# Kernel tuning notes

Hardware: AMD Instinct MI355X
Metric: run time of the kernel (lower is better)

The kernel has to match this reference:

```python
import jax, jax.numpy as jnp
import numpy as np

H = 256
K = 16
EPS_LN = 1e-5


def setup_inputs() -> dict:
    key = jax.random.key(0)
    ks = jax.random.split(key, 24)
    B, N = 64, 256
    s = lambda *sh: 1.0 / np.sqrt(sh[0])
    inp = {
        "feat": jax.random.normal(ks[0], (B, N, H), jnp.float32),
        "centers": jax.random.normal(ks[1], (B, N, 3), jnp.float32),
        "text_global": jax.random.normal(ks[2], (B, H), jnp.float32),
        # geom_mlp: Linear(4,H) -> ReLU -> Linear(H,H) -> ReLU
        "w_geom1": jax.random.normal(ks[3], (4, H), jnp.float32) * s(4),
        "b_geom1": jnp.zeros((H,), jnp.float32),
        "w_geom2": jax.random.normal(ks[4], (H, H), jnp.float32) * s(H),
        "b_geom2": jnp.zeros((H,), jnp.float32),
        # text gate / bias projections
        "w_gate": jax.random.normal(ks[5], (H, H), jnp.float32) * s(H),
        "b_gate": jnp.zeros((H,), jnp.float32),
        "w_tbias": jax.random.normal(ks[6], (H, H), jnp.float32) * s(H),
        "b_tbias": jnp.zeros((H,), jnp.float32),
        # edge_mlp: Linear(H,H//2) -> ReLU -> Linear(H//2,1)
        "w_edge1": jax.random.normal(ks[7], (H, H // 2), jnp.float32) * s(H),
        "b_edge1": jnp.zeros((H // 2,), jnp.float32),
        "w_edge2": jax.random.normal(ks[8], (H // 2, 1), jnp.float32) * s(H // 2),
        "b_edge2": jnp.zeros((1,), jnp.float32),
        # msg_mlp: Linear(H,H) -> ReLU
        "w_msg": jax.random.normal(ks[9], (H, H), jnp.float32) * s(H),
        "b_msg": jnp.zeros((H,), jnp.float32),
        # out_proj: Linear(2H,H) -> ReLU
        "w_out": jax.random.normal(ks[10], (2 * H, H), jnp.float32) * s(2 * H),
        "b_out": jnp.zeros((H,), jnp.float32),
        # LayerNorm params
        "ln_gamma": jnp.ones((H,), jnp.float32),
        "ln_beta": jnp.zeros((H,), jnp.float32),
    }
    return inp


def _forward(feat, centers, text_global,
             w_geom1, b_geom1, w_geom2, b_geom2,
             w_gate, b_gate, w_tbias, b_tbias,
             w_edge1, b_edge1, w_edge2, b_edge2,
             w_msg, b_msg, w_out, b_out, ln_gamma, ln_beta):
    B, N, Hd = feat.shape
    k = min(K, N)
    # pairwise euclidean distances (B,N,N)
    sq = jnp.sum(centers * centers, axis=-1)  # (B,N)
    d2 = sq[:, :, None] + sq[:, None, :] - 2.0 * jnp.einsum('bnc,bmc->bnm', centers, centers)
    dist_matrix = jnp.sqrt(jnp.maximum(d2, 0.0))
    # k smallest -> top_k of negated distances (sorted ascending in distance)
    _, knn_idx = jax.lax.top_k(-dist_matrix, k)  # (B,N,k)
    idx_flat = knn_idx.reshape(B, N * k)
    feat_neigh = jnp.take_along_axis(feat, idx_flat[:, :, None], axis=1).reshape(B, N, k, Hd)
    centers_neigh = jnp.take_along_axis(centers, idx_flat[:, :, None], axis=1).reshape(B, N, k, 3)
    rel = centers_neigh - centers[:, :, None, :]  # (B,N,k,3)
    dist = jnp.linalg.norm(rel, axis=-1, keepdims=True) + 1e-6
    geom = jnp.concatenate([rel, jnp.log1p(dist)], axis=-1)  # (B,N,k,4)
    geom_emb = jax.nn.relu(jax.nn.relu(geom @ w_geom1 + b_geom1) @ w_geom2 + b_geom2)
    text_gate = jax.nn.sigmoid(text_global @ w_gate + b_gate)[:, None, None, :]
    text_bias = (text_global @ w_tbias + b_tbias)[:, None, None, :]
    geom_cond = geom_emb * text_gate + text_bias
    edge_feat = jnp.tanh(feat[:, :, None, :] + feat_neigh + geom_cond)  # (B,N,k,H)
    edge_logits = (jax.nn.relu(edge_feat @ w_edge1 + b_edge1) @ w_edge2 + b_edge2)[..., 0]
    edge_alpha = jax.nn.softmax(edge_logits, axis=-1)[..., None]  # (B,N,k,1)
    msg = jax.nn.relu(feat_neigh @ w_msg + b_msg)
    ctx = jnp.sum(edge_alpha * msg, axis=2)  # (B,N,H)
    out = jax.nn.relu(jnp.concatenate([feat, ctx], axis=-1) @ w_out + b_out)
    x = feat + out
    mu = jnp.mean(x, axis=-1, keepdims=True)
    var = jnp.mean((x - mu) ** 2, axis=-1, keepdims=True)
    return (x - mu) / jnp.sqrt(var + EPS_LN) * ln_gamma + ln_beta


def reference(feat, centers, text_global,
              w_geom1, b_geom1, w_geom2, b_geom2,
              w_gate, b_gate, w_tbias, b_tbias,
              w_edge1, b_edge1, w_edge2, b_edge2,
              w_msg, b_msg, w_out, b_out, ln_gamma, ln_beta):
    return _forward(feat, centers, text_global,
                    w_geom1, b_geom1, w_geom2, b_geom2,
                    w_gate, b_gate, w_tbias, b_tbias,
                    w_edge1, b_edge1, w_edge2, b_edge2,
                    w_msg, b_msg, w_out, b_out, ln_gamma, ln_beta)
```

## Files before the change

### kernel.cpp

```cpp
#include <hip/hip_runtime.h>
#include <hip/hip_bf16.h>

#define H 256
#define KNN 16
#define NPT 256
#define BB 64

typedef unsigned short u16;
typedef unsigned int u32;
typedef __attribute__((ext_vector_type(8))) short shortx8;
typedef __attribute__((ext_vector_type(4))) float floatx4;

__device__ __forceinline__ u16 f2b(float f) {
    return __builtin_bit_cast(u16, __float2bfloat16(f));
}
__device__ __forceinline__ float b2f(u16 u) {
    return __uint_as_float(((u32)u) << 16);
}

__device__ __forceinline__ float fast_tanh(float x) {
    float e = __builtin_amdgcn_exp2f(x * 2.88539008177793f);
    return 1.0f - 2.0f * __builtin_amdgcn_rcpf(e + 1.0f);
}

__global__ __launch_bounds__(256) void prep_kernel(
    const float* __restrict__ w2, const float* __restrict__ we1,
    const float* __restrict__ wm, const float* __restrict__ wo,
    const float* __restrict__ w1, const float* __restrict__ b1,
    u16* __restrict__ w2t, u16* __restrict__ we1t,
    u16* __restrict__ wmt, u16* __restrict__ wot, u16* __restrict__ w1t) {
    int tid = blockIdx.x * 256 + threadIdx.x;
    if (tid < 65536) {
        int n = tid >> 8, k = tid & 255;
        w2t[tid] = f2b(w2[k * 256 + n]);
    } else if (tid < 98304) {
        int t = tid - 65536;
        int n = t >> 8, k = t & 255;
        we1t[t] = f2b(we1[k * 128 + n]);
    } else if (tid < 163840) {
        int t = tid - 98304;
        int n = t >> 8, k = t & 255;
        wmt[t] = f2b(wm[k * 256 + n]);
    } else if (tid < 294912) {
        int t = tid - 163840;
        int n = t >> 9, k = t & 511;
        wot[t] = f2b(wo[k * 256 + n]);
    } else {
        int t = tid - 294912;
        int n = t >> 5, k = t & 31;
        float v = (k < 4) ? w1[k * 256 + n] : (k == 4 ? b1[n] : 0.0f);
        w1t[t] = f2b(v);
    }
}

__global__ __launch_bounds__(256) void knn_kernel(const float* __restrict__ centers,
                                                  int* __restrict__ knn) {
    __shared__ float cx[NPT], cy[NPT], cz[NPT], sq[NPT];
    __shared__ float dl[4][64][17];
    __shared__ int il[4][64][17];
    int blk = blockIdx.x;
    int b = blk >> 2, n0 = (blk & 3) * 64;
    int h = threadIdx.x;
    int s = h >> 6, pt = h & 63;
    {
        const float* cb = centers + (size_t)b * NPT * 3;
        float x = cb[h * 3 + 0], y = cb[h * 3 + 1], z = cb[h * 3 + 2];
        cx[h] = x; cy[h] = y; cz[h] = z;
        sq[h] = x * x + y * y + z * z;
    }
    __syncthreads();
    int n = n0 + pt;
    float x = cx[n], y = cy[n], z = cz[n], sn = sq[n];
    float bd[KNN];
    int bi[KNN];
#pragma unroll
    for (int j = 0; j < KNN; j++) { bd[j] = 1e30f; bi[j] = 0x7fffffff; }
    for (int mm = 0; mm < 64; mm++) {
        int m = s * 64 + mm;
        float dot = x * cx[m] + y * cy[m] + z * cz[m];
        float d2 = (sn + sq[m]) - 2.0f * dot;
        float d = sqrtf(fmaxf(d2, 0.0f));
        if (d < bd[KNN - 1]) {
            bd[KNN - 1] = d; bi[KNN - 1] = m;
#pragma unroll
            for (int p = KNN - 1; p > 0; --p) {
                if (bd[p - 1] > bd[p]) {
                    float td = bd[p - 1]; bd[p - 1] = bd[p]; bd[p] = td;
                    int ti = bi[p - 1]; bi[p - 1] = bi[p]; bi[p] = ti;
                }
            }
        }
    }
#pragma unroll
    for (int j = 0; j < KNN; j++) { dl[s][pt][j] = bd[j]; il[s][pt][j] = bi[j]; }
    __syncthreads();
    if (s == 0) {
        float md[KNN];
        int mi[KNN];
#pragma unroll
        for (int j = 0; j < KNN; j++) { md[j] = dl[0][pt][j]; mi[j] = il[0][pt][j]; }
        for (int t = 1; t < 4; t++) {
            for (int j = 0; j < KNN; j++) {
                float d = dl[t][pt][j];
                int idx = il[t][pt][j];
                bool ins = (d < md[KNN - 1]) || (d == md[KNN - 1] && idx < mi[KNN - 1]);
                if (!ins) break;
                md[KNN - 1] = d; mi[KNN - 1] = idx;
#pragma unroll
                for (int p = KNN - 1; p > 0; --p) {
                    bool sw = (md[p - 1] > md[p]) ||
                              (md[p - 1] == md[p] && mi[p - 1] > mi[p]);
                    if (sw) {
                        float td = md[p - 1]; md[p - 1] = md[p]; md[p] = td;
                        int ti = mi[p - 1]; mi[p - 1] = mi[p]; mi[p] = ti;
                    }
                }
            }
        }
        int* kp = knn + (b * NPT + n0 + pt) * KNN;
#pragma unroll
        for (int j = 0; j < KNN; j++) kp[j] = mi[j];
    }
}

__global__ __launch_bounds__(512) void gate_kernel(const float* __restrict__ tg_g,
                                                   const float* __restrict__ wg,
                                                   const float* __restrict__ bg,
                                                   const float* __restrict__ wtb,
                                                   const float* __restrict__ btb,
                                                   float* __restrict__ gate,
                                                   float* __restrict__ tbias) {
    __shared__ float tg[H];
    int b = blockIdx.x, t = threadIdx.x;
    if (t < H) tg[t] = tg_g[b * H + t];
    __syncthreads();
    int h = t & 255;
    if (t < H) {
        float ag = bg[h];
#pragma unroll 4
        for (int i = 0; i < H; i++) ag += tg[i] * wg[i * H + h];
        gate[b * H + h] = 1.0f / (1.0f + expf(-ag));
    } else {
        float ab = btb[h];
#pragma unroll 4
        for (int i = 0; i < H; i++) ab += tg[i] * wtb[i * H + h];
        tbias[b * H + h] = ab;
    }
}

__global__ __launch_bounds__(256, 4) void msg_mfma(const float* __restrict__ feat,
                                                   const u16* __restrict__ wmt,
                                                   const float* __restrict__ bm,
                                                   u16* __restrict__ MSGB,
                                                   u16* __restrict__ featB) {
    __shared__ __attribute__((aligned(16))) u16 A[64][264];
    int p0 = blockIdx.x * 64, h = threadIdx.x;
    int w = h >> 6, lane = h & 63, quad = lane >> 4, lq = lane & 15;
#pragma unroll 8
    for (int row = 0; row < 64; row++) {
        u16 v = f2b(feat[(size_t)(p0 + row) * H + h]);
        A[row][h] = v;
        featB[(size_t)(p0 + row) * H + h] = v;
    }
    __syncthreads();
    floatx4 acc[4][4];
#pragma unroll
    for (int rt = 0; rt < 4; rt++)
#pragma unroll
        for (int ct = 0; ct < 4; ct++) acc[rt][ct] = (floatx4){0, 0, 0, 0};
#pragma unroll 2
    for (int kt = 0; kt < 8; kt++) {
        shortx8 bf[4];
#pragma unroll
        for (int ct = 0; ct < 4; ct++)
            bf[ct] = *(const shortx8*)&wmt[(w * 64 + ct * 16 + lq) * 256 + kt * 32 + quad * 8];
#pragma unroll
        for (int rt = 0; rt < 4; rt++) {
            shortx8 a = *(const shortx8*)&A[rt * 16 + lq][kt * 32 + quad * 8];
#pragma unroll
            for (int ct = 0; ct < 4; ct++)
                acc[rt][ct] = __builtin_amdgcn_mfma_f32_16x16x32_bf16(a, bf[ct], acc[rt][ct], 0, 0, 0);
        }
    }
#pragma unroll
    for (int ct = 0; ct < 4; ct++) {
        int col = w * 64 + ct * 16 + lq;
        float bmc = bm[col];
#pragma unroll
        for (int rt = 0; rt < 4; rt++)
#pragma unroll
            for (int r = 0; r < 4; r++) {
                int row = rt * 16 + quad * 4 + r;
                MSGB[(size_t)(p0 + row) * H + col] = f2b(fmaxf(acc[rt][ct][r] + bmc, 0.0f));
            }
    }
}

__global__ __launch_bounds__(256, 4) void edge_mfma(
    const float* __restrict__ feat, const u16* __restrict__ featB,
    const float* __restrict__ centers,
    const u16* __restrict__ w1t,
    const u16* __restrict__ w2t, const float* __restrict__ b2v,
    const u16* __restrict__ we1t, const float* __restrict__ be1,
    const float* __restrict__ we2, const float* __restrict__ be2,
    const int* __restrict__ knn, const float* __restrict__ gateG,
    const float* __restrict__ tbiasG, const u16* __restrict__ MSGB,
    u16* __restrict__ ctxB) {
    __shared__ __attribute__((aligned(16))) u16 A[64][264];
    __shared__ float fnS[4][H];
    __shared__ __attribute__((aligned(16))) float geomS[64][4];
    __shared__ int nidxS[64];
    __shared__ float part[4][64];
    __shared__ float logitsS[64];
    __shared__ float alphaS[64];

    int bn0 = blockIdx.x * 4;
    int b = bn0 >> 8, n0 = bn0 & 255;
    int h = threadIdx.x;
    int w = h >> 6, lane = h & 63, quad = lane >> 4, lq = lane & 15;

    if (h < 64) nidxS[h] = knn[bn0 * KNN + h];
#pragma unroll
    for (int p = 0; p < 4; p++)
        fnS[p][h] = feat[(size_t)(bn0 + p) * H + h];
    if (h < 64) {
        int p = h >> 4;
        int m = nidxS[h];
        int n = n0 + p;
        const float* cb = centers + (size_t)b * NPT * 3;
        float rx = cb[m * 3 + 0] - cb[n * 3 + 0];
        float ry = cb[m * 3 + 1] - cb[n * 3 + 1];
        float rz = cb[m * 3 + 2] - cb[n * 3 + 2];
        float dist = sqrtf(rx * rx + ry * ry + rz * rz) + 1e-6f;
        geomS[h][0] = rx; geomS[h][1] = ry; geomS[h][2] = rz;
        geomS[h][3] = log1pf(dist);
    }
    __syncthreads();

    {
        shortx8 bw1[4];
#pragma unroll
        for (int ct = 0; ct < 4; ct++)
            bw1[ct] = *(const shortx8*)&w1t[(w * 64 + ct * 16 + lq) * 32 + quad * 8];
#pragma unroll
        for (int rt = 0; rt < 4; rt++) {
            shortx8 ag = {0, 0, 0, 0, 0, 0, 0, 0};
            if (quad == 0) {
                float4 g = *(const float4*)&geomS[rt * 16 + lq][0];
                ag[0] = (short)f2b(g.x);
                ag[1] = (short)f2b(g.y);
                ag[2] = (short)f2b(g.z);
                ag[3] = (short)f2b(g.w);
                ag[4] = (short)0x3F80;
            }
#pragma unroll
            for (int ct = 0; ct < 4; ct++) {
                floatx4 accg = __builtin_amdgcn_mfma_f32_16x16x32_bf16(
                    ag, bw1[ct], (floatx4){0, 0, 0, 0}, 0, 0, 0);
#pragma unroll
                for (int r = 0; r < 4; r++)
                    A[rt * 16 + quad * 4 + r][w * 64 + ct * 16 + lq] =
                        f2b(fmaxf(accg[r], 0.0f));
            }
        }
    }
    __syncthreads();

    floatx4 acc[4][4];
#pragma unroll
    for (int rt = 0; rt < 4; rt++)
#pragma unroll
        for (int ct = 0; ct < 4; ct++) acc[rt][ct] = (floatx4){0, 0, 0, 0};
#pragma unroll 2
    for (int kt = 0; kt < 8; kt++) {
        shortx8 bf[4];
#pragma unroll
        for (int ct = 0; ct < 4; ct++)
            bf[ct] = *(const shortx8*)&w2t[(w * 64 + ct * 16 + lq) * 256 + kt * 32 + quad * 8];
#pragma unroll
        for (int rt = 0; rt < 4; rt++) {
            shortx8 a = *(const shortx8*)&A[rt * 16 + lq][kt * 32 + quad * 8];
#pragma unroll
            for (int ct = 0; ct < 4; ct++)
                acc[rt][ct] = __builtin_amdgcn_mfma_f32_16x16x32_bf16(a, bf[ct], acc[rt][ct], 0, 0, 0);
        }
    }
    __syncthreads();

#pragma unroll
    for (int ct = 0; ct < 4; ct++) {
        int col = w * 64 + ct * 16 + lq;
        float b2c = b2v[col];
        float gc = gateG[b * H + col];
        float tc = tbiasG[b * H + col];
#pragma unroll
        for (int rt = 0; rt < 4; rt++) {
            float fnc = fnS[rt][col];
#pragma unroll
            for (int r = 0; r < 4; r++) {
                int row = rt * 16 + quad * 4 + r;
                float fb = b2f(featB[((size_t)b * NPT + nidxS[row]) * H + col]);
                float emb = fmaxf(acc[rt][ct][r] + b2c, 0.0f);
                float ef = fast_tanh(fnc + fb + emb * gc + tc);
                A[row][col] = f2b(ef);
            }
        }
    }
    __syncthreads();

    floatx4 acc2[4][2];
#pragma unroll
    for (int rt = 0; rt < 4; rt++)
#pragma unroll
        for (int c2 = 0; c2 < 2; c2++) acc2[rt][c2] = (floatx4){0, 0, 0, 0};
#pragma unroll 2
    for (int kt = 0; kt < 8; kt++) {
        shortx8 bf[2];
#pragma unroll
        for (int c2 = 0; c2 < 2; c2++)
            bf[c2] = *(const shortx8*)&we1t[(w * 32 + c2 * 16 + lq) * 256 + kt * 32 + quad * 8];
#pragma unroll
        for (int rt = 0; rt < 4; rt++) {
            shortx8 a = *(const shortx8*)&A[rt * 16 + lq][kt * 32 + quad * 8];
#pragma unroll
            for (int c2 = 0; c2 < 2; c2++)
                acc2[rt][c2] = __builtin_amdgcn_mfma_f32_16x16x32_bf16(a, bf[c2], acc2[rt][c2], 0, 0, 0);
        }
    }

    float pl[4][4];
#pragma unroll
    for (int rt = 0; rt < 4; rt++)
#pragma unroll
        for (int r = 0; r < 4; r++) pl[rt][r] = 0.0f;
#pragma unroll
    for (int c2 = 0; c2 < 2; c2++) {
        int col = w * 32 + c2 * 16 + lq;
        float be1c = be1[col], w2c = we2[col];
#pragma unroll
        for (int rt = 0; rt < 4; rt++)
#pragma unroll
            for (int r = 0; r < 4; r++)
                pl[rt][r] += fmaxf(acc2[rt][c2][r] + be1c, 0.0f) * w2c;
    }
#pragma unroll
    for (int d = 1; d < 16; d <<= 1)
#pragma unroll
        for (int rt = 0; rt < 4; rt++)
#pragma unroll
            for (int r = 0; r < 4; r++) pl[rt][r] += __shfl_xor(pl[rt][r], d, 16);
    if (lq == 0) {
#pragma unroll
        for (int rt = 0; rt < 4; rt++)
#pragma unroll
            for (int r = 0; r < 4; r++)
                part[w][rt * 16 + quad * 4 + r] = pl[rt][r];
    }
    __syncthreads();
    if (h < 64)
        logitsS[h] = part[0][h] + part[1][h] + part[2][h] + part[3][h] + be2[0];
    __syncthreads();
    if (h < 64) {
        int base = (h >> 4) * 16;
        float mx = -1e30f;
#pragma unroll
        for (int j = 0; j < KNN; j++) mx = fmaxf(mx, logitsS[base + j]);
        float sum = 0.0f;
#pragma unroll
        for (int j = 0; j < KNN; j++) sum += expf(logitsS[base + j] - mx);
        alphaS[h] = expf(logitsS[h] - mx) / sum;
    }
    __syncthreads();

    {
        int p = h >> 6, cg = (h & 63) * 4;
        float4 c = {0, 0, 0, 0};
#pragma unroll
        for (int j = 0; j < KNN; j++) {
            float al = alphaS[p * 16 + j];
            const u32* mp = (const u32*)&MSGB[((size_t)b * NPT + nidxS[p * 16 + j]) * H + cg];
            u32 m0 = mp[0], m1 = mp[1];
            c.x += al * __uint_as_float(m0 << 16);
            c.y += al * __uint_as_float(m0 & 0xFFFF0000u);
            c.z += al * __uint_as_float(m1 << 16);
            c.w += al * __uint_as_float(m1 & 0xFFFF0000u);
        }
        uint2 st;
        st.x = (u32)f2b(c.x) | ((u32)f2b(c.y) << 16);
        st.y = (u32)f2b(c.z) | ((u32)f2b(c.w) << 16);
        *(uint2*)&ctxB[(size_t)(bn0 + p) * H + cg] = st;
    }
}

__global__ __launch_bounds__(256, 4) void out_mfma(const float* __restrict__ feat,
                                                   const u16* __restrict__ featB,
                                                   const u16* __restrict__ ctxB,
                                                   const u16* __restrict__ wot,
                                                   const float* __restrict__ bo,
                                                   const float* __restrict__ gamma,
                                                   const float* __restrict__ beta,
                                                   float* __restrict__ out) {
    __shared__ __attribute__((aligned(16))) u16 A[32][520];
    __shared__ float redS[4][32], redS2[4][32];
    int p0 = blockIdx.x * 32, h = threadIdx.x;
    int w = h >> 6, lane = h & 63, quad = lane >> 4, lq = lane & 15;
#pragma unroll 8
    for (int row = 0; row < 32; row++) {
        A[row][h]       = featB[(size_t)(p0 + row) * H + h];
        A[row][256 + h] = ctxB[(size_t)(p0 + row) * H + h];
    }
    __syncthreads();
    floatx4 acc[2][4];
#pragma unroll
    for (int rt = 0; rt < 2; rt++)
#pragma unroll
        for (int ct = 0; ct < 4; ct++) acc[rt][ct] = (floatx4){0, 0, 0, 0};
#pragma unroll 2
    for (int kt = 0; kt < 16; kt++) {
        shortx8 bf[4];
#pragma unroll
        for (int ct = 0; ct < 4; ct++)
            bf[ct] = *(const shortx8*)&wot[(w * 64 + ct * 16 + lq) * 512 + kt * 32 + quad * 8];
#pragma unroll
        for (int rt = 0; rt < 2; rt++) {
            shortx8 a = *(const shortx8*)&A[rt * 16 + lq][kt * 32 + quad * 8];
#pragma unroll
            for (int ct = 0; ct < 4; ct++)
                acc[rt][ct] = __builtin_amdgcn_mfma_f32_16x16x32_bf16(a, bf[ct], acc[rt][ct], 0, 0, 0);
        }
    }
    float x[2][4][4];
    float sm[2][4], sq2[2][4];
#pragma unroll
    for (int rt = 0; rt < 2; rt++)
#pragma unroll
        for (int r = 0; r < 4; r++) { sm[rt][r] = 0.0f; sq2[rt][r] = 0.0f; }
#pragma unroll
    for (int rt = 0; rt < 2; rt++)
#pragma unroll
        for (int ct = 0; ct < 4; ct++) {
            int col = w * 64 + ct * 16 + lq;
            float boc = bo[col];
#pragma unroll
            for (int r = 0; r < 4; r++) {
                int row = rt * 16 + quad * 4 + r;
                float xx = feat[(size_t)(p0 + row) * H + col] +
                           fmaxf(acc[rt][ct][r] + boc, 0.0f);
                x[rt][ct][r] = xx;
                sm[rt][r] += xx;
                sq2[rt][r] += xx * xx;
            }
        }
#pragma unroll
    for (int d = 1; d < 16; d <<= 1)
#pragma unroll
        for (int rt = 0; rt < 2; rt++)
#pragma unroll
            for (int r = 0; r < 4; r++) {
                sm[rt][r] += __shfl_xor(sm[rt][r], d, 16);
                sq2[rt][r] += __shfl_xor(sq2[rt][r], d, 16);
            }
    if (lq == 0) {
#pragma unroll
        for (int rt = 0; rt < 2; rt++)
#pragma unroll
            for (int r = 0; r < 4; r++) {
                redS[w][rt * 16 + quad * 4 + r] = sm[rt][r];
                redS2[w][rt * 16 + quad * 4 + r] = sq2[rt][r];
            }
    }
    __syncthreads();
#pragma unroll
    for (int rt = 0; rt < 2; rt++)
#pragma unroll
        for (int r = 0; r < 4; r++) {
            int row = rt * 16 + quad * 4 + r;
            float s1 = redS[0][row] + redS[1][row] + redS[2][row] + redS[3][row];
            float s2 = redS2[0][row] + redS2[1][row] + redS2[2][row] + redS2[3][row];
            float mu = s1 * (1.0f / H);
            float var = s2 * (1.0f / H) - mu * mu;
            float inv = rsqrtf(fmaxf(var, 0.0f) + 1e-5f);
#pragma unroll
            for (int ct = 0; ct < 4; ct++) {
                int col = w * 64 + ct * 16 + lq;
                out[(size_t)(p0 + row) * H + col] =
                    (x[rt][ct][r] - mu) * inv * gamma[col] + beta[col];
            }
        }
}

extern "C" void kernel_launch(void* const* d_in, const int* in_sizes, int n_in,
                              void* d_out, int out_size, void* d_ws, size_t ws_size,
                              hipStream_t stream) {
    const float* feat    = (const float*)d_in[0];
    const float* centers = (const float*)d_in[1];
    const float* textg   = (const float*)d_in[2];
    const float* w1      = (const float*)d_in[3];
    const float* b1      = (const float*)d_in[4];
    const float* w2      = (const float*)d_in[5];
    const float* b2      = (const float*)d_in[6];
    const float* wg      = (const float*)d_in[7];
    const float* bg      = (const float*)d_in[8];
    const float* wtb     = (const float*)d_in[9];
    const float* btb     = (const float*)d_in[10];
    const float* we1     = (const float*)d_in[11];
    const float* be1     = (const float*)d_in[12];
    const float* we2     = (const float*)d_in[13];
    const float* be2     = (const float*)d_in[14];
    const float* wm      = (const float*)d_in[15];
    const float* bm      = (const float*)d_in[16];
    const float* wo      = (const float*)d_in[17];
    const float* bo      = (const float*)d_in[18];
    const float* gamma   = (const float*)d_in[19];
    const float* beta    = (const float*)d_in[20];

    char* ws = (char*)d_ws;
    size_t off = 0;
    int* knn     = (int*)(ws + off);   off += (size_t)BB * NPT * KNN * 4;
    float* gate  = (float*)(ws + off); off += (size_t)BB * H * 4;
    float* tbias = (float*)(ws + off); off += (size_t)BB * H * 4;
    u16* MSGB    = (u16*)(ws + off);   off += (size_t)BB * NPT * H * 2;
    u16* ctxB    = (u16*)(ws + off);   off += (size_t)BB * NPT * H * 2;
    u16* featB   = (u16*)(ws + off);   off += (size_t)BB * NPT * H * 2;
    u16* w2t     = (u16*)(ws + off);   off += (size_t)256 * 256 * 2;
    u16* we1t    = (u16*)(ws + off);   off += (size_t)128 * 256 * 2;
    u16* wmt     = (u16*)(ws + off);   off += (size_t)256 * 256 * 2;
    u16* wot     = (u16*)(ws + off);   off += (size_t)256 * 512 * 2;
    u16* w1t     = (u16*)(ws + off);   off += (size_t)256 * 32 * 2;

    prep_kernel<<<1184, 256, 0, stream>>>(w2, we1, wm, wo, w1, b1,
                                          w2t, we1t, wmt, wot, w1t);
    knn_kernel<<<256, 256, 0, stream>>>(centers, knn);
    gate_kernel<<<BB, 512, 0, stream>>>(textg, wg, bg, wtb, btb, gate, tbias);
    msg_mfma<<<BB * NPT / 64, 256, 0, stream>>>(feat, wmt, bm, MSGB, featB);
    edge_mfma<<<BB * NPT / 4, 256, 0, stream>>>(feat, featB, centers, w1t, w2t, b2,
                                                we1t, be1, we2, be2, knn, gate, tbias,
                                                MSGB, ctxB);
    out_mfma<<<BB * NPT / 32, 256, 0, stream>>>(feat, featB, ctxB, wot, bo,
                                                gamma, beta, (float*)d_out);
}
```

Before: 347.1 us.

## Stage neighbor gathers into swizzled LDS via async global_load_lds

Replaces the padded LDS tile with an XOR-swizzled unpadded layout. It then uses direct global-to-LDS loads to stage the gathered neighbor featB rows and MSGB rows into that buffer before they are consumed. This replaces scattered per-element 2-byte global gathers with coalesced 16-byte row loads. The MSGB prefetch is issued before the softmax, so its latency can overlap that work. Correctness depends on the swizzle being applied consistently and on the async LDS writes being complete before the buffer is read.

Result: slower. 358.6 us (+3.3%).

```diff
diff --git a/kernel.cpp b/kernel.cpp
--- a/kernel.cpp
+++ b/kernel.cpp
@@ -21,6 +21,16 @@
 __device__ __forceinline__ float fast_tanh(float x) {
     float e = __builtin_amdgcn_exp2f(x * 2.88539008177793f);
     return 1.0f - 2.0f * __builtin_amdgcn_rcpf(e + 1.0f);
+}
+
+__device__ __forceinline__ int aoff(int row, int col) {
+    return (row << 8) + ((((col >> 3) ^ (row & 7)) << 3) | (col & 7));
+}
+
+__device__ __forceinline__ void gload_lds16(const u16* g, u16* l) {
+    __builtin_amdgcn_global_load_lds(
+        (const __attribute__((address_space(1))) unsigned int*)g,
+        (__attribute__((address_space(3))) unsigned int*)l, 16, 0, 0);
 }
 
 __global__ __launch_bounds__(256) void prep_kernel(
@@ -206,7 +216,7 @@
     const int* __restrict__ knn, const float* __restrict__ gateG,
     const float* __restrict__ tbiasG, const u16* __restrict__ MSGB,
     u16* __restrict__ ctxB) {
-    __shared__ __attribute__((aligned(16))) u16 A[64][264];
+    __shared__ __attribute__((aligned(16))) u16 A[64 * 256];
     __shared__ float fnS[4][H];
     __shared__ __attribute__((aligned(16))) float geomS[64][4];
     __shared__ int nidxS[64];
@@ -259,7 +269,7 @@
                     ag, bw1[ct], (floatx4){0, 0, 0, 0}, 0, 0, 0);
 #pragma unroll
                 for (int r = 0; r < 4; r++)
-                    A[rt * 16 + quad * 4 + r][w * 64 + ct * 16 + lq] =
+                    A[aoff(rt * 16 + quad * 4 + r, w * 64 + ct * 16 + lq)] =
                         f2b(fmaxf(accg[r], 0.0f));
             }
         }
@@ -279,10 +289,23 @@
             bf[ct] = *(const shortx8*)&w2t[(w * 64 + ct * 16 + lq) * 256 + kt * 32 + quad * 8];
 #pragma unroll
         for (int rt = 0; rt < 4; rt++) {
-            shortx8 a = *(const shortx8*)&A[rt * 16 + lq][kt * 32 + quad * 8];
+            shortx8 a = *(const shortx8*)&A[((rt * 16 + lq) << 8) +
+                                            (((kt * 4 + quad) ^ (lq & 7)) << 3)];
 #pragma unroll
             for (int ct = 0; ct < 4; ct++)
                 acc[rt][ct] = __builtin_amdgcn_mfma_f32_16x16x32_bf16(a, bf[ct], acc[rt][ct], 0, 0, 0);
+        }
+    }
+    __syncthreads();
+
+    {
+        size_t bbase = (size_t)b * NPT;
+#pragma unroll
+        for (int i = 0; i < 8; i++) {
+            int R = (w << 4) + 2 * i + (lane >> 5);
+            const u16* src = featB + (bbase + nidxS[R]) * H +
+                             (((lane & 31) ^ (R & 7)) << 3);
+            gload_lds16(src, &A[((w << 4) + 2 * i) << 8]);
         }
     }
     __syncthreads();
@@ -295,14 +318,14 @@
         float tc = tbiasG[b * H + col];
 #pragma unroll
         for (int rt = 0; rt < 4; rt++) {
-            float fnc = fnS[rt][col];
+            float fnt = fnS[rt][col] + tc;
 #pragma unroll
             for (int r = 0; r < 4; r++) {
                 int row = rt * 16 + quad * 4 + r;
-                float fb = b2f(featB[((size_t)b * NPT + nidxS[row]) * H + col]);
+                int off = aoff(row, col);
+                float fb = b2f(A[off]);
                 float emb = fmaxf(acc[rt][ct][r] + b2c, 0.0f);
-                float ef = fast_tanh(fnc + fb + emb * gc + tc);
-                A[row][col] = f2b(ef);
+                A[off] = f2b(fast_tanh(fnt + fb + emb * gc));
             }
         }
     }
@@ -321,7 +344,8 @@
             bf[c2] = *(const shortx8*)&we1t[(w * 32 + c2 * 16 + lq) * 256 + kt * 32 + quad * 8];
 #pragma unroll
         for (int rt = 0; rt < 4; rt++) {
-            shortx8 a = *(const shortx8*)&A[rt * 16 + lq][kt * 32 + quad * 8];
+            shortx8 a = *(const shortx8*)&A[((rt * 16 + lq) << 8) +
+                                            (((kt * 4 + quad) ^ (lq & 7)) << 3)];
 #pragma unroll
             for (int c2 = 0; c2 < 2; c2++)
                 acc2[rt][c2] = __builtin_amdgcn_mfma_f32_16x16x32_bf16(a, bf[c2], acc2[rt][c2], 0, 0, 0);
@@ -357,6 +381,17 @@
                 part[w][rt * 16 + quad * 4 + r] = pl[rt][r];
     }
     __syncthreads();
+
+    {
+        size_t bbase = (size_t)b * NPT;
+#pragma unroll
+        for (int i = 0; i < 8; i++) {
+            int R = (w << 4) + 2 * i + (lane >> 5);
+            const u16* src = MSGB + (bbase + nidxS[R]) * H +
+                             (((lane & 31) ^ (R & 7)) << 3);
+            gload_lds16(src, &A[((w << 4) + 2 * i) << 8]);
+        }
+    }
     if (h < 64)
         logitsS[h] = part[0][h] + part[1][h] + part[2][h] + part[3][h] + be2[0];
     __syncthreads();
@@ -377,13 +412,14 @@
         float4 c = {0, 0, 0, 0};
 #pragma unroll
         for (int j = 0; j < KNN; j++) {
-            float al = alphaS[p * 16 + j];
-            const u32* mp = (const u32*)&MSGB[((size_t)b * NPT + nidxS[p * 16 + j]) * H + cg];
-            u32 m0 = mp[0], m1 = mp[1];
-            c.x += al * __uint_as_float(m0 << 16);
-            c.y += al * __uint_as_float(m0 & 0xFFFF0000u);
-            c.z += al * __uint_as_float(m1 << 16);
-            c.w += al * __uint_as_float(m1 & 0xFFFF0000u);
+            int row = p * 16 + j;
+            float al = alphaS[row];
+            uint2 m = *(const uint2*)&A[(row << 8) +
+                                        ((((cg >> 3) ^ (row & 7)) << 3) | (cg & 7))];
+            c.x += al * __uint_as_float(m.x << 16);
+            c.y += al * __uint_as_float(m.x & 0xFFFF0000u);
+            c.z += al * __uint_as_float(m.y << 16);
+            c.w += al * __uint_as_float(m.y & 0xFFFF0000u);
         }
         uint2 st;
         st.x = (u32)f2b(c.x) | ((u32)f2b(c.y) << 16);
```

## Halve edge kernel tile to two points per block and raise occupancy

Applied to the files above, without the earlier changes.

The edge kernel now handles 2 points (32 edges) per block instead of 4 (64 edges), doubling the grid, and launch bounds move from 4 to 6 blocks per CU. The smaller accumulator arrays and per-iteration weight loads are meant to cut register and LDS use so more waves fit per CU and hide gather latency. In exchange, each block re-reads the w2t/we1t weights with half as many rows to amortise them over, so there is less reuse. Minor tweaks fold the text bias into the feature term and narrow the context gather to two channels per thread.

Result: slower. 439.2 us (+26.5%).

```diff
diff --git a/kernel.cpp b/kernel.cpp
--- a/kernel.cpp
+++ b/kernel.cpp
@@ -196,7 +196,7 @@
     }
 }
 
-__global__ __launch_bounds__(256, 4) void edge_mfma(
+__global__ __launch_bounds__(256, 6) void edge_mfma(
     const float* __restrict__ feat, const u16* __restrict__ featB,
     const float* __restrict__ centers,
     const u16* __restrict__ w1t,
@@ -206,24 +206,24 @@
     const int* __restrict__ knn, const float* __restrict__ gateG,
     const float* __restrict__ tbiasG, const u16* __restrict__ MSGB,
     u16* __restrict__ ctxB) {
-    __shared__ __attribute__((aligned(16))) u16 A[64][264];
-    __shared__ float fnS[4][H];
-    __shared__ __attribute__((aligned(16))) float geomS[64][4];
-    __shared__ int nidxS[64];
-    __shared__ float part[4][64];
-    __shared__ float logitsS[64];
-    __shared__ float alphaS[64];
-
-    int bn0 = blockIdx.x * 4;
+    __shared__ __attribute__((aligned(16))) u16 A[32][264];
+    __shared__ float fnS[2][H];
+    __shared__ __attribute__((aligned(16))) float geomS[32][4];
+    __shared__ int nidxS[32];
+    __shared__ float part[4][32];
+    __shared__ float logitsS[32];
+    __shared__ float alphaS[32];
+
+    int bn0 = blockIdx.x * 2;
     int b = bn0 >> 8, n0 = bn0 & 255;
     int h = threadIdx.x;
     int w = h >> 6, lane = h & 63, quad = lane >> 4, lq = lane & 15;
 
-    if (h < 64) nidxS[h] = knn[bn0 * KNN + h];
-#pragma unroll
-    for (int p = 0; p < 4; p++)
+    if (h < 32) nidxS[h] = knn[bn0 * KNN + h];
+#pragma unroll
+    for (int p = 0; p < 2; p++)
         fnS[p][h] = feat[(size_t)(bn0 + p) * H + h];
-    if (h < 64) {
+    if (h < 32) {
         int p = h >> 4;
         int m = nidxS[h];
         int n = n0 + p;
@@ -238,12 +238,8 @@
     __syncthreads();
 
     {
-        shortx8 bw1[4];
-#pragma unroll
-        for (int ct = 0; ct < 4; ct++)
-            bw1[ct] = *(const shortx8*)&w1t[(w * 64 + ct * 16 + lq) * 32 + quad * 8];
-#pragma unroll
-        for (int rt = 0; rt < 4; rt++) {
+#pragma unroll
+        for (int rt = 0; rt < 2; rt++) {
             shortx8 ag = {0, 0, 0, 0, 0, 0, 0, 0};
             if (quad == 0) {
                 float4 g = *(const float4*)&geomS[rt * 16 + lq][0];
@@ -255,8 +251,9 @@
             }
 #pragma unroll
             for (int ct = 0; ct < 4; ct++) {
+                shortx8 bw1 = *(const shortx8*)&w1t[(w * 64 + ct * 16 + lq) * 32 + quad * 8];
                 floatx4 accg = __builtin_amdgcn_mfma_f32_16x16x32_bf16(
-                    ag, bw1[ct], (floatx4){0, 0, 0, 0}, 0, 0, 0);
+                    ag, bw1, (floatx4){0, 0, 0, 0}, 0, 0, 0);
 #pragma unroll
                 for (int r = 0; r < 4; r++)
                     A[rt * 16 + quad * 4 + r][w * 64 + ct * 16 + lq] =
@@ -266,23 +263,19 @@
     }
     __syncthreads();
 
-    floatx4 acc[4][4];
-#pragma unroll
-    for (int rt = 0; rt < 4; rt++)
+    floatx4 acc[2][4];
+#pragma unroll
+    for (int rt = 0; rt < 2; rt++)
 #pragma unroll
         for (int ct = 0; ct < 4; ct++) acc[rt][ct] = (floatx4){0, 0, 0, 0};
-#pragma unroll 2
     for (int kt = 0; kt < 8; kt++) {
-        shortx8 bf[4];
-#pragma unroll
-        for (int ct = 0; ct < 4; ct++)
-            bf[ct] = *(const shortx8*)&w2t[(w * 64 + ct * 16 + lq) * 256 + kt * 32 + quad * 8];
-#pragma unroll
-        for (int rt = 0; rt < 4; rt++) {
-            shortx8 a = *(const shortx8*)&A[rt * 16 + lq][kt * 32 + quad * 8];
-#pragma unroll
-            for (int ct = 0; ct < 4; ct++)
-                acc[rt][ct] = __builtin_amdgcn_mfma_f32_16x16x32_bf16(a, bf[ct], acc[rt][ct], 0, 0, 0);
+        shortx8 a0 = *(const shortx8*)&A[lq][kt * 32 + quad * 8];
+        shortx8 a1 = *(const shortx8*)&A[16 + lq][kt * 32 + quad * 8];
+#pragma unroll
+        for (int ct = 0; ct < 4; ct++) {
+            shortx8 bf = *(const shortx8*)&w2t[(w * 64 + ct * 16 + lq) * 256 + kt * 32 + quad * 8];
+            acc[0][ct] = __builtin_amdgcn_mfma_f32_16x16x32_bf16(a0, bf, acc[0][ct], 0, 0, 0);
+            acc[1][ct] = __builtin_amdgcn_mfma_f32_16x16x32_bf16(a1, bf, acc[1][ct], 0, 0, 0);
         }
     }
     __syncthreads();
@@ -294,43 +287,39 @@
         float gc = gateG[b * H + col];
         float tc = tbiasG[b * H + col];
 #pragma unroll
-        for (int rt = 0; rt < 4; rt++) {
-            float fnc = fnS[rt][col];
+        for (int rt = 0; rt < 2; rt++) {
+            float fnt = fnS[rt][col] + tc;
 #pragma unroll
             for (int r = 0; r < 4; r++) {
                 int row = rt * 16 + quad * 4 + r;
                 float fb = b2f(featB[((size_t)b * NPT + nidxS[row]) * H + col]);
                 float emb = fmaxf(acc[rt][ct][r] + b2c, 0.0f);
-                float ef = fast_tanh(fnc + fb + emb * gc + tc);
+                float ef = fast_tanh(fnt + fb + emb * gc);
                 A[row][col] = f2b(ef);
             }
         }
     }
     __syncthreads();
 
-    floatx4 acc2[4][2];
-#pragma unroll
-    for (int rt = 0; rt < 4; rt++)
+    floatx4 acc2[2][2];
+#pragma unroll
+    for (int rt = 0; rt < 2; rt++)
 #pragma unroll
         for (int c2 = 0; c2 < 2; c2++) acc2[rt][c2] = (floatx4){0, 0, 0, 0};
-#pragma unroll 2
     for (int kt = 0; kt < 8; kt++) {
-        shortx8 bf[2];
-#pragma unroll
-        for (int c2 = 0; c2 < 2; c2++)
-            bf[c2] = *(const shortx8*)&we1t[(w * 32 + c2 * 16 + lq) * 256 + kt * 32 + quad * 8];
-#pragma unroll
-        for (int rt = 0; rt < 4; rt++) {
-            shortx8 a = *(const shortx8*)&A[rt * 16 + lq][kt * 32 + quad * 8];
-#pragma unroll
-            for (int c2 = 0; c2 < 2; c2++)
-                acc2[rt][c2] = __builtin_amdgcn_mfma_f32_16x16x32_bf16(a, bf[c2], acc2[rt][c2], 0, 0, 0);
-        }
-    }
-
-    float pl[4][4];
-#pragma unroll
-    for (int rt = 0; rt < 4; rt++)
+        shortx8 a0 = *(const shortx8*)&A[lq][kt * 32 + quad * 8];
+        shortx8 a1 = *(const shortx8*)&A[16 + lq][kt * 32 + quad * 8];
+#pragma unroll
+        for (int c2 = 0; c2 < 2; c2++) {
+            shortx8 bf = *(const shortx8*)&we1t[(w * 32 + c2 * 16 + lq) * 256 + kt * 32 + quad * 8];
+            acc2[0][c2] = __builtin_amdgcn_mfma_f32_16x16x32_bf16(a0, bf, acc2[0][c2], 0, 0, 0);
+            acc2[1][c2] = __builtin_amdgcn_mfma_f32_16x16x32_bf16(a1, bf, acc2[1][c2], 0, 0, 0);
+        }
+    }
+
+    float pl[2][4];
+#pragma unroll
+    for (int rt = 0; rt < 2; rt++)
 #pragma unroll
         for (int r = 0; r < 4; r++) pl[rt][r] = 0.0f;
 #pragma unroll
@@ -338,7 +327,7 @@
         int col = w * 32 + c2 * 16 + lq;
         float be1c = be1[col], w2c = we2[col];
 #pragma unroll
-        for (int rt = 0; rt < 4; rt++)
+        for (int rt = 0; rt < 2; rt++)
 #pragma unroll
             for (int r = 0; r < 4; r++)
                 pl[rt][r] += fmaxf(acc2[rt][c2][r] + be1c, 0.0f) * w2c;
@@ -346,21 +335,21 @@
 #pragma unroll
     for (int d = 1; d < 16; d <<= 1)
 #pragma unroll
-        for (int rt = 0; rt < 4; rt++)
+        for (int rt = 0; rt < 2; rt++)
 #pragma unroll
             for (int r = 0; r < 4; r++) pl[rt][r] += __shfl_xor(pl[rt][r], d, 16);
     if (lq == 0) {
 #pragma unroll
-        for (int rt = 0; rt < 4; rt++)
+        for (int rt = 0; rt < 2; rt++)
 #pragma unroll
             for (int r = 0; r < 4; r++)
                 part[w][rt * 16 + quad * 4 + r] = pl[rt][r];
     }
     __syncthreads();
-    if (h < 64)
+    if (h < 32)
         logitsS[h] = part[0][h] + part[1][h] + part[2][h] + part[3][h] + be2[0];
     __syncthreads();
-    if (h < 64) {
+    if (h < 32) {
         int base = (h >> 4) * 16;
         float mx = -1e30f;
 #pragma unroll
@@ -373,22 +362,18 @@
     __syncthreads();
 
     {
-        int p = h >> 6, cg = (h & 63) * 4;
-        float4 c = {0, 0, 0, 0};
+        int p = h >> 7, cg = (h & 127) * 2;
+        float cx = 0.0f, cy = 0.0f;
 #pragma unroll
         for (int j = 0; j < KNN; j++) {
-            float al = alphaS[p * 16 + j];
-            const u32* mp = (const u32*)&MSGB[((size_t)b * NPT + nidxS[p * 16 + j]) * H + cg];
-            u32 m0 = mp[0], m1 = mp[1];
-            c.x += al * __uint_as_float(m0 << 16);
-            c.y += al * __uint_as_float(m0 & 0xFFFF0000u);
-            c.z += al * __uint_as_float(m1 << 16);
-            c.w += al * __uint_as_float(m1 & 0xFFFF0000u);
-        }
-        uint2 st;
-        st.x = (u32)f2b(c.x) | ((u32)f2b(c.y) << 16);
-        st.y = (u32)f2b(c.z) | ((u32)f2b(c.w) << 16);
-        *(uint2*)&ctxB[(size_t)(bn0 + p) * H + cg] = st;
+            int row = p * 16 + j;
+            float al = alphaS[row];
+            u32 m0 = *(const u32*)&MSGB[((size_t)b * NPT + nidxS[row]) * H + cg];
+            cx += al * __uint_as_float(m0 << 16);
+            cy += al * __uint_as_float(m0 & 0xFFFF0000u);
+        }
+        u32 st = (u32)f2b(cx) | ((u32)f2b(cy) << 16);
+        *(u32*)&ctxB[(size_t)(bn0 + p) * H + cg] = st;
     }
 }
 
@@ -533,7 +518,7 @@
     knn_kernel<<<256, 256, 0, stream>>>(centers, knn);
     gate_kernel<<<BB, 512, 0, stream>>>(textg, wg, bg, wtb, btb, gate, tbias);
     msg_mfma<<<BB * NPT / 64, 256, 0, stream>>>(feat, wmt, bm, MSGB, featB);
-    edge_mfma<<<BB * NPT / 4, 256, 0, stream>>>(feat, featB, centers, w1t, w2t, b2,
+    edge_mfma<<<BB * NPT / 2, 256, 0, stream>>>(feat, featB, centers, w1t, w2t, b2,
                                                 we1t, be1, we2, be2, knn, gate, tbias,
                                                 MSGB, ctxB);
     out_mfma<<<BB * NPT / 32, 256, 0, stream>>>(feat, featB, ctxB, wot, bo,
```
